# Kernel optimization log

Measured on AMD Instinct MI355X. Metric: run time of the kernel, lower is better.

The kernel has to match this reference:

```python
import jax, jax.numpy as jnp
import numpy as np

HEADS = 24
R = 4          # vae_time_compression_ratio
WIN = 3        # windows_size
PAD_T = R * WIN
ROPE_DIMS = (24, 4, 4)   # mouse_qk_dim_list, sum == head_dim == 32
THETA = 256.0
EPS = 1e-6


def setup_inputs():
    key = jax.random.key(0)
    ks = jax.random.split(key, 8)
    b, tt, th, tw = 2, 16, 30, 52
    C = 768
    head_dim = C // HEADS
    mouse_dim, kb_dim = 2, 6
    nf = (tt - 1) * R + 1          # raw frames so feature_time_dim == tt
    in_mlp = mouse_dim * PAD_T + C
    s = 0.02
    return {
        "mouse_condition": jax.random.normal(ks[0], (b, nf, mouse_dim), jnp.float32),
        "keyboard_condition": jax.random.normal(ks[1], (b, nf, kb_dim), jnp.float32),
        "x": jax.random.normal(ks[2], (b, tt * th * tw, C), jnp.float32),
        "mlp_w1": jax.random.normal(ks[3], (in_mlp, in_mlp), jnp.float32) * s,
        "mlp_b1": jnp.zeros((in_mlp,), jnp.float32),
        "mlp_w2": jax.random.normal(ks[4], (in_mlp, C), jnp.float32) * s,
        "mlp_b2": jnp.zeros((C,), jnp.float32),
        "qkv_w": jax.random.normal(ks[5], (C, 3 * C), jnp.float32) * s,
        "q_gamma": jnp.ones((head_dim,), jnp.float32),
        "k_gamma": jnp.ones((head_dim,), jnp.float32),
        "proj_w": jax.random.normal(ks[6], (C, C), jnp.float32) * s,
        "tt": 16, "th": 30, "tw": 52,
    }


def _rms_norm(x, gamma):
    return x * jax.lax.rsqrt(jnp.mean(x * x, -1, keepdims=True) + EPS) * gamma


def _rope_freqs(tt, head_dim):
    # 3-axis rope, rope_sizes = (tt, 1, 1): axes 1 and 2 have position 0 (identity).
    pos = [jnp.arange(tt, dtype=jnp.float32),
           jnp.zeros(tt, jnp.float32),
           jnp.zeros(tt, jnp.float32)]
    cos_l, sin_l = [], []
    for d, p in zip(ROPE_DIMS, pos):
        freqs = 1.0 / (THETA ** (jnp.arange(0, d, 2, dtype=jnp.float32) / d))
        ang = jnp.outer(p, freqs)                      # (tt, d//2)
        cos_l.append(jnp.repeat(jnp.cos(ang), 2, axis=1))   # interleaved convention
        sin_l.append(jnp.repeat(jnp.sin(ang), 2, axis=1))
    return jnp.concatenate(cos_l, -1), jnp.concatenate(sin_l, -1)  # (tt, head_dim)


def _rotate_half(x):
    xr = x.reshape(*x.shape[:-1], -1, 2)
    return jnp.stack([-xr[..., 1], xr[..., 0]], -1).reshape(x.shape)


def reference(mouse_condition, keyboard_condition, x, mlp_w1, mlp_b1, mlp_w2, mlp_b2,
              qkv_w, q_gamma, k_gamma, proj_w, tt, th, tw):
    b, L, C = x.shape
    S = th * tw
    head_dim = C // HEADS
    md = mouse_condition.shape[-1]

    # 'B (T S) C -> (B S) T C'
    hs = x.reshape(b, tt, S, C).transpose(0, 2, 1, 3).reshape(b * S, tt, C)

    # sliding windows over front-padded mouse signal: stride R, window PAD_T
    mp = jnp.pad(mouse_condition, ((0, 0), (PAD_T, 0), (0, 0)))
    idx = R * jnp.arange(tt)[:, None] + jnp.arange(PAD_T)[None, :]
    gm = mp[:, idx, :].reshape(b, 1, tt, PAD_T * md)          # (window, d) flattened
    gm = jnp.broadcast_to(gm, (b, S, tt, PAD_T * md)).reshape(b * S, tt, PAD_T * md)

    z = jnp.concatenate([hs, gm], -1)
    h = jax.nn.gelu(z @ mlp_w1 + mlp_b1, approximate=True)    # gelu_tanh
    feat = h @ mlp_w2 + mlp_b2                                # (b*S, tt, C)

    qkv = (feat @ qkv_w).reshape(b * S, tt, 3, HEADS, head_dim)
    q, k, v = qkv[:, :, 0], qkv[:, :, 1], qkv[:, :, 2]
    q = _rms_norm(q, q_gamma)
    k = _rms_norm(k, k_gamma)

    cos, sin = _rope_freqs(tt, head_dim)
    cos = cos[None, :, None, :]
    sin = sin[None, :, None, :]
    q = q * cos + _rotate_half(q) * sin
    k = k * cos + _rotate_half(k) * sin

    scale = head_dim ** -0.5
    scores = jnp.einsum('blhd,bmhd->bhlm', q, k) * scale
    p = jax.nn.softmax(scores, axis=-1)
    attn = jnp.einsum('bhlm,bmhd->blhd', p, v).reshape(b * S, tt, C)

    # '(b S) T h d -> b (T S) (h d)'
    attn = attn.reshape(b, S, tt, C).transpose(0, 2, 1, 3).reshape(b, tt * S, C)
    return x + attn @ proj_w
```

## Files before the change

### kernel.cpp

```cpp
#include <hip/hip_runtime.h>

typedef unsigned short u16;
typedef __bf16 bf16x8 __attribute__((ext_vector_type(8)));
typedef float f32x4 __attribute__((ext_vector_type(4)));
typedef short short8 __attribute__((ext_vector_type(8)));

#define TT 16
#define SP 1560
#define CDIM 768
#define NHEADS 24
#define KP 800
#define HROWS 896
#define HSTR 800

__device__ __forceinline__ float b2f(u16 u){
  unsigned int x = ((unsigned int)u) << 16;
  return __builtin_bit_cast(float, x);
}
__device__ __forceinline__ u16 f2b(float f){
  unsigned int x = __builtin_bit_cast(unsigned int, f);
  x += 0x7fffu + ((x >> 16) & 1u);
  return (u16)(x >> 16);
}
__device__ __forceinline__ float ldf(const void* p, size_t i, int f32){
  return f32 ? ((const float*)p)[i] : b2f(((const u16*)p)[i]);
}
__device__ __forceinline__ void g2l16(const void* g, void* l){
  __builtin_amdgcn_global_load_lds((const __attribute__((address_space(1))) void*)g,
                                   (__attribute__((address_space(3))) void*)l, 16, 0, 0);
}

__global__ void detect_dtype(const u16* __restrict__ x, int* __restrict__ flag){
  __shared__ int sh[256];
  int tid = threadIdx.x;
  int cnt = 0;
  #pragma unroll
  for (int j=0;j<8;j++){
    u16 u = x[(size_t)(tid*8+j)*2];
    int e = (u >> 7) & 0xff;
    cnt += (e >= 90 && e <= 160) ? 1 : 0;
  }
  sh[tid] = cnt;
  __syncthreads();
  if (tid == 0){
    int s = 0;
    for (int k=0;k<256;k++) s += sh[k];
    *flag = (s < 1024) ? 1 : 0;
  }
}

__global__ void convert(const void* __restrict__ src, u16* __restrict__ dst,
                        int n, const int* __restrict__ flagp){
  int f = *flagp;
  int i = blockIdx.x*256 + threadIdx.x;
  int stride = gridDim.x*256;
  if (f){
    const float* s = (const float*)src;
    for (int j=i; j<n; j+=stride) dst[j] = f2b(s[j]);
  } else {
    const u16* s = (const u16*)src;
    for (int j=i; j<n; j+=stride) dst[j] = s[j];
  }
}

__global__ void build_gm(const void* __restrict__ mouse, u16* __restrict__ gm,
                         int b, const int* __restrict__ flagp){
  int f = *flagp;
  int i = blockIdx.x*256 + threadIdx.x;
  if (i >= b*TT*32) return;
  int col = i & 31, tix = i >> 5;
  int t = tix & 15, bidx = tix >> 4;
  float v = 0.f;
  if (col < 24){
    int j = col >> 1, c = col & 1;
    int p = 4*t + j;
    if (p >= 12) v = ldf(mouse, (size_t)(bidx*61 + (p-12))*2 + c, f);
  }
  gm[i] = f2b(v);
}

__global__ void transpose_pad(const void* __restrict__ src, u16* __restrict__ dst,
                              int K, int N, int Kpad, int Npad,
                              const int* __restrict__ flagp){
  int f = *flagp;
  __shared__ u16 tile[32][33];
  int k0 = blockIdx.x*32, n0 = blockIdx.y*32;
  int tx = threadIdx.x, ty = threadIdx.y;
  #pragma unroll
  for (int i=0;i<32;i+=8){
    int k = k0+ty+i, n = n0+tx;
    u16 v = 0;
    if (k<K && n<N) v = f ? f2b(((const float*)src)[(size_t)k*N+n])
                          : ((const u16*)src)[(size_t)k*N+n];
    tile[ty+i][tx] = v;
  }
  __syncthreads();
  #pragma unroll
  for (int i=0;i<32;i+=8){
    int n = n0+ty+i, k = k0+tx;
    if (n<Npad && k<Kpad) dst[(size_t)n*Kpad+k] = tile[tx][ty+i];
  }
}

template<int AMODE, int EPI>
__global__ __launch_bounds__(256, 4) void gemm(
    const u16* __restrict__ A, int lda,
    const u16* __restrict__ Bt, int ldb, int Kpad,
    const u16* __restrict__ bias,
    const u16* __restrict__ X,
    const u16* __restrict__ gmtab,
    u16* __restrict__ C, u16* __restrict__ Ck, u16* __restrict__ Cv,
    int ldc, int nmax,
    const int* __restrict__ flagp)
{
  __shared__ __attribute__((aligned(16))) u16 As[2][128*32];
  __shared__ __attribute__((aligned(16))) u16 Bs[2][128*32];
  int f32out = 0;
  if constexpr (EPI==3) f32out = *flagp;

  const int gx = gridDim.x;
  const int nwg = gx * gridDim.y;
  const int orig = blockIdx.y * gx + blockIdx.x;
  const int q8 = nwg >> 3, r8 = nwg & 7;
  const int xcd = orig & 7, idx = orig >> 3;
  const int nl = (xcd < r8 ? xcd*(q8+1) : r8*(q8+1) + (xcd-r8)*q8) + idx;
  const int bx = nl % gx, by = nl / gx;

  const int tid = threadIdx.x;
  const int wave = tid >> 6, lane = tid & 63;
  const int lrow = lane & 15, quad = lane >> 4;
  const int m0 = by * 128, n0 = bx * 128;
  const int wm = (wave >> 1) * 64, wn = (wave & 1) * 64;
  const int row = tid >> 2;
  const int kc  = (tid & 3) << 3;

  f32x4 acc[4][4];
  #pragma unroll
  for (int r=0;r<4;r++)
    #pragma unroll
    for (int c=0;c<4;c++) acc[r][c] = (f32x4){0.f,0.f,0.f,0.f};

  auto STAGE = [&](int bi, int k0){
    #pragma unroll
    for (int ch=0; ch<2; ch++){
      int m = m0 + ch*64 + row;
      const u16* srcA;
      if (AMODE==1 && k0 >= CDIM) srcA = gmtab + (m/SP)*32 + (k0 - CDIM) + kc;
      else                        srcA = A + (size_t)m*lda + k0 + kc;
      g2l16(srcA, (char*)(&As[bi][0]) + ch*4096 + wave*1024);
      int n = n0 + ch*64 + row;
      const u16* srcB = Bt + (size_t)n*ldb + k0 + kc;
      g2l16(srcB, (char*)(&Bs[bi][0]) + ch*4096 + wave*1024);
    }
  };

  auto COMPUTE = [&](int bi){
    bf16x8 af[4], bfr[4];
    #pragma unroll
    for (int r=0;r<4;r++) af[r]  = *(const bf16x8*)&As[bi][(wm + r*16 + lrow)*32 + quad*8];
    #pragma unroll
    for (int c=0;c<4;c++) bfr[c] = *(const bf16x8*)&Bs[bi][(wn + c*16 + lrow)*32 + quad*8];
    #pragma unroll
    for (int r=0;r<4;r++)
      #pragma unroll
      for (int c=0;c<4;c++)
        acc[r][c] = __builtin_amdgcn_mfma_f32_16x16x32_bf16(af[r], bfr[c], acc[r][c], 0, 0, 0);
  };

  const int nt = Kpad >> 5;
  STAGE(0, 0);
  __syncthreads();
  int cur = 0;
  for (int t = 0; t < nt-1; ++t){
    STAGE(cur^1, (t+1) << 5);
    COMPUTE(cur);
    __syncthreads();
    cur ^= 1;
  }
  COMPUTE(cur);

  #pragma unroll
  for (int c=0;c<4;c++){
    int n = n0 + wn + c*16 + lrow;
    float bv = 0.f;
    if (EPI==1) bv = (n < 792) ? b2f(bias[n]) : 0.f;
    if (EPI==2) bv = b2f(bias[n]);
    u16* dstb = C;
    int nn = n;
    if constexpr (EPI==4){
      int sec = n / 768;
      nn = n - sec*768;
      dstb = (sec==0) ? C : ((sec==1) ? Ck : Cv);
    }
    #pragma unroll
    for (int r=0;r<4;r++){
      #pragma unroll
      for (int i=0;i<4;i++){
        int m = m0 + wm + r*16 + quad*4 + i;
        float v = acc[r][c][i] + bv;
        if (EPI==1){
          float u = 0.7978845608028654f*(v + 0.044715f*v*v*v);
          v = 0.5f*v*(1.f + tanhf(u));
        }
        if (EPI==3) v += b2f(X[(size_t)m*CDIM + n]);
        if (n < nmax){
          if constexpr (EPI==3){
            if (f32out) ((float*)C)[(size_t)m*ldc + n] = v;
            else        C[(size_t)m*ldc + n] = f2b(v);
          } else {
            dstb[(size_t)m*ldc + nn] = f2b(v);
          }
        }
      }
    }
  }
}

__global__ __launch_bounds__(256) void attn_kernel(
    const u16* __restrict__ qp, const u16* __restrict__ kp,
    const u16* __restrict__ vp, const u16* __restrict__ qg,
    const u16* __restrict__ kg, u16* __restrict__ outp)
{
  __shared__ float qs[4][16][32];
  __shared__ float ks[4][16][32];
  __shared__ float vs[4][16][32];
  __shared__ float ps[4][16][16];
  const int tid = threadIdx.x;
  const int wave = tid >> 6, lane = tid & 63;
  const int inst = blockIdx.x*4 + wave;
  const int head = inst % NHEADS;
  const int bs   = inst / NHEADS;
  const int s = bs % SP, bidx = bs / SP;
  const int t = lane >> 2, ch = lane & 3;
  const size_t mrow = (size_t)(bidx*TT + t)*SP + s;
  const size_t off = mrow*CDIM + head*32 + ch*8;

  float qf[8], kf[8], vf[8];
  {
    short8 r0 = *(const short8*)(qp + off);
    short8 r1 = *(const short8*)(kp + off);
    short8 r2 = *(const short8*)(vp + off);
    #pragma unroll
    for (int j=0;j<8;j++){ qf[j]=b2f((u16)r0[j]); kf[j]=b2f((u16)r1[j]); vf[j]=b2f((u16)r2[j]); }
  }
  float ssq=0.f, ssk=0.f;
  #pragma unroll
  for (int j=0;j<8;j++){ ssq += qf[j]*qf[j]; ssk += kf[j]*kf[j]; }
  ssq += __shfl_xor(ssq,1); ssq += __shfl_xor(ssq,2);
  ssk += __shfl_xor(ssk,1); ssk += __shfl_xor(ssk,2);
  float rq = rsqrtf(ssq*(1.f/32.f) + 1e-6f);
  float rk = rsqrtf(ssk*(1.f/32.f) + 1e-6f);
  #pragma unroll
  for (int j=0;j<8;j++){
    int d = ch*8 + j;
    qf[j] *= rq * b2f(qg[d]);
    kf[j] *= rk * b2f(kg[d]);
  }
  #pragma unroll
  for (int u=0;u<4;u++){
    int p = ch*4 + u;
    if (p < 12){
      float ang = (float)t * exp2f(-0.66666667f * (float)p);
      float sn, cs;
      __sincosf(ang, &sn, &cs);
      float a=qf[2*u], b=qf[2*u+1];
      qf[2*u]   = a*cs - b*sn;
      qf[2*u+1] = b*cs + a*sn;
      a=kf[2*u]; b=kf[2*u+1];
      kf[2*u]   = a*cs - b*sn;
      kf[2*u+1] = b*cs + a*sn;
    }
  }
  #pragma unroll
  for (int j=0;j<8;j++){
    qs[wave][t][ch*8+j]=qf[j];
    ks[wave][t][ch*8+j]=kf[j];
    vs[wave][t][ch*8+j]=vf[j];
  }
  __syncthreads();
  float sc[4]; float mx = -3.4e38f;
  #pragma unroll
  for (int jj=0;jj<4;jj++){
    int j = ch*4 + jj;
    float d = 0.f;
    #pragma unroll
    for (int dd=0;dd<32;dd++) d += qs[wave][t][dd]*ks[wave][j][dd];
    sc[jj] = d * 0.17677669529663689f;
    mx = fmaxf(mx, sc[jj]);
  }
  mx = fmaxf(mx, __shfl_xor(mx,1)); mx = fmaxf(mx, __shfl_xor(mx,2));
  float sum=0.f; float ex[4];
  #pragma unroll
  for (int jj=0;jj<4;jj++){ ex[jj]=__expf(sc[jj]-mx); sum+=ex[jj]; }
  sum += __shfl_xor(sum,1); sum += __shfl_xor(sum,2);
  float inv = 1.f/sum;
  #pragma unroll
  for (int jj=0;jj<4;jj++) ps[wave][t][ch*4+jj] = ex[jj]*inv;
  __syncthreads();
  float o[8] = {0,0,0,0,0,0,0,0};
  #pragma unroll
  for (int j=0;j<16;j++){
    float p = ps[wave][t][j];
    #pragma unroll
    for (int dd=0;dd<8;dd++) o[dd] += p * vs[wave][j][ch*8+dd];
  }
  union { short8 v; u16 u[8]; } pk;
  #pragma unroll
  for (int dd=0;dd<8;dd++) pk.u[dd] = f2b(o[dd]);
  *(short8*)(outp + off) = pk.v;
}

extern "C" void kernel_launch(void* const* d_in, const int* in_sizes, int n_in,
                              void* d_out, int out_size, void* d_ws, size_t ws_size,
                              hipStream_t stream){
  const void* mouse = d_in[0];
  const void* x     = d_in[2];
  const void* w1    = d_in[3];
  const void* b1    = d_in[4];
  const void* w2    = d_in[5];
  const void* b2    = d_in[6];
  const void* qkvw  = d_in[7];
  const void* qg    = d_in[8];
  const void* kg    = d_in[9];
  const void* projw = d_in[10];
  const int b = in_sizes[0] / (61*2);
  const int M = b * TT * SP;

  u16* ws    = (u16*)d_ws;
  int* flag  = (int*)ws;
  u16* gm    = ws + 32;
  u16* bcvt  = gm + 1024;
  u16* b1b   = bcvt;
  u16* b2b   = bcvt + 800;
  u16* qgb   = bcvt + 1568;
  u16* kgb   = bcvt + 1600;
  u16* w1t   = bcvt + 2048;
  u16* w2t   = w1t  + (size_t)HROWS*KP;
  u16* qkvt  = w2t  + (size_t)CDIM*KP;
  u16* projt = qkvt + (size_t)(3*CDIM)*CDIM;
  u16* xb    = projt+ (size_t)CDIM*CDIM;
  u16* h     = xb   + (size_t)M*CDIM;
  u16* feat  = h    + (size_t)M*HSTR;
  u16* kbuf  = feat + (size_t)M*CDIM;
  u16* vbuf  = kbuf + (size_t)M*CDIM;
  u16* qbuf  = h;
  u16* attn  = feat;

  detect_dtype<<<1, 256, 0, stream>>>((const u16*)x, flag);
  convert<<<dim3(4),    256, 0, stream>>>(b1, b1b, 792, flag);
  convert<<<dim3(3),    256, 0, stream>>>(b2, b2b, 768, flag);
  convert<<<dim3(1),    256, 0, stream>>>(qg, qgb, 32, flag);
  convert<<<dim3(1),    256, 0, stream>>>(kg, kgb, 32, flag);
  convert<<<dim3(8192), 256, 0, stream>>>(x,  xb,  M*CDIM, flag);
  build_gm<<<dim3((b*TT*32+255)/256), 256, 0, stream>>>(mouse, gm, b, flag);
  dim3 tb(32,8);
  transpose_pad<<<dim3(KP/32,   HROWS/32),    tb, 0, stream>>>(w1,   w1t,   792,  792,    KP,   HROWS, flag);
  transpose_pad<<<dim3(KP/32,   CDIM/32),     tb, 0, stream>>>(w2,   w2t,   792,  CDIM,   KP,   CDIM,  flag);
  transpose_pad<<<dim3(CDIM/32, (3*CDIM)/32), tb, 0, stream>>>(qkvw, qkvt,  CDIM, 3*CDIM, CDIM, 3*CDIM,flag);
  transpose_pad<<<dim3(CDIM/32, CDIM/32),     tb, 0, stream>>>(projw, projt, CDIM, CDIM,  CDIM, CDIM,  flag);

  gemm<1,1><<<dim3(HROWS/128, M/128), 256, 0, stream>>>(xb,   CDIM, w1t,  KP,   KP,   b1b, nullptr, gm,
                                                        h,    nullptr, nullptr, HSTR, 800, flag);
  gemm<0,2><<<dim3(CDIM/128,  M/128), 256, 0, stream>>>(h,    HSTR, w2t,  KP,   KP,   b2b, nullptr, nullptr,
                                                        feat, nullptr, nullptr, CDIM, 768, flag);
  gemm<0,4><<<dim3((3*CDIM)/128, M/128), 256, 0, stream>>>(feat, CDIM, qkvt, CDIM, CDIM, nullptr, nullptr, nullptr,
                                                           qbuf, kbuf, vbuf, CDIM, 3*CDIM, flag);
  attn_kernel<<<dim3(b*SP*NHEADS/4), 256, 0, stream>>>(qbuf, kbuf, vbuf, qgb, kgb, attn);
  gemm<0,3><<<dim3(CDIM/128,  M/128), 256, 0, stream>>>(attn, CDIM, projt, CDIM, CDIM, nullptr, xb, nullptr,
                                                        (u16*)d_out, nullptr, nullptr, CDIM, 768, flag);
}
```

Measured before the change: 1.058 ms.

## Replace 128x128 GEMM with 256x256 tiled, swizzled, phase-pipelined GEMM

Replaces the 128x128x32 double-buffered GEMM with a 512-thread 256x256x64 tile kernel. It uses XOR-swizzled LDS layout, four-phase interleaving of half-tile loads with MFMA work, and setprio around the compute. K padding grows to 896, N padding for the first GEMM to 1024, and the gm table widens to 128 columns to fit the 64-wide K steps. The goal is more data reuse per LDS load and fewer bank conflicts and stalls, at the cost of larger padding waste and lower occupancy.

Result: slower. 1.209 ms (+14.2%).

```diff
diff --git a/kernel.cpp b/kernel.cpp
--- a/kernel.cpp
+++ b/kernel.cpp
@@ -9,9 +9,9 @@
 #define SP 1560
 #define CDIM 768
 #define NHEADS 24
-#define KP 800
-#define HROWS 896
-#define HSTR 800
+#define KP1 896
+#define HSTR 896
+#define N1PAD 1024
 
 __device__ __forceinline__ float b2f(u16 u){
   unsigned int x = ((unsigned int)u) << 16;
@@ -67,8 +67,8 @@
                          int b, const int* __restrict__ flagp){
   int f = *flagp;
   int i = blockIdx.x*256 + threadIdx.x;
-  if (i >= b*TT*32) return;
-  int col = i & 31, tix = i >> 5;
+  if (i >= b*TT*128) return;
+  int col = i & 127, tix = i >> 7;
   int t = tix & 15, bidx = tix >> 4;
   float v = 0.f;
   if (col < 24){
@@ -103,7 +103,7 @@
 }
 
 template<int AMODE, int EPI>
-__global__ __launch_bounds__(256, 4) void gemm(
+__global__ __launch_bounds__(512, 2) void gemm256(
     const u16* __restrict__ A, int lda,
     const u16* __restrict__ Bt, int ldb, int Kpad,
     const u16* __restrict__ bias,
@@ -113,10 +113,8 @@
     int ldc, int nmax,
     const int* __restrict__ flagp)
 {
-  __shared__ __attribute__((aligned(16))) u16 As[2][128*32];
-  __shared__ __attribute__((aligned(16))) u16 Bs[2][128*32];
-  int f32out = 0;
-  if constexpr (EPI==3) f32out = *flagp;
+  __shared__ __attribute__((aligned(16))) u16 sA[2][256*64];
+  __shared__ __attribute__((aligned(16))) u16 sB[2][256*64];
 
   const int gx = gridDim.x;
   const int nwg = gx * gridDim.y;
@@ -128,60 +126,109 @@
 
   const int tid = threadIdx.x;
   const int wave = tid >> 6, lane = tid & 63;
-  const int lrow = lane & 15, quad = lane >> 4;
-  const int m0 = by * 128, n0 = bx * 128;
-  const int wm = (wave >> 1) * 64, wn = (wave & 1) * 64;
-  const int row = tid >> 2;
-  const int kc  = (tid & 3) << 3;
-
-  f32x4 acc[4][4];
-  #pragma unroll
-  for (int r=0;r<4;r++)
+  const int wm8 = wave >> 2, wn8 = wave & 3;
+  const int lrow = lane & 15, hi16 = lane >> 4;
+  const int m0 = by*256, n0 = bx*256;
+
+  f32x4 acc[8][4];
+  #pragma unroll
+  for (int r=0;r<8;r++)
     #pragma unroll
     for (int c=0;c<4;c++) acc[r][c] = (f32x4){0.f,0.f,0.f,0.f};
 
-  auto STAGE = [&](int bi, int k0){
-    #pragma unroll
-    for (int ch=0; ch<2; ch++){
-      int m = m0 + ch*64 + row;
-      const u16* srcA;
-      if (AMODE==1 && k0 >= CDIM) srcA = gmtab + (m/SP)*32 + (k0 - CDIM) + kc;
-      else                        srcA = A + (size_t)m*lda + k0 + kc;
-      g2l16(srcA, (char*)(&As[bi][0]) + ch*4096 + wave*1024);
-      int n = n0 + ch*64 + row;
-      const u16* srcB = Bt + (size_t)n*ldb + k0 + kc;
-      g2l16(srcB, (char*)(&Bs[bi][0]) + ch*4096 + wave*1024);
+  const int nt = Kpad >> 6;
+  const int niter = nt >> 1;
+
+  auto STAGE = [&](int isB, int buf, int half, int k0){
+    #pragma unroll
+    for (int is=0; is<2; is++){
+      int r = half*128 + is*64 + (tid>>3);
+      int ck = (((tid&7) ^ (r&7)) << 3);
+      const u16* src;
+      if (isB){
+        src = Bt + (size_t)(n0 + r)*ldb + k0 + ck;
+      } else {
+        int m = m0 + r;
+        if (AMODE==1 && k0 >= CDIM) src = gmtab + (size_t)(m/SP)*128 + (k0 - CDIM) + ck;
+        else                        src = A + (size_t)m*lda + k0 + ck;
+      }
+      char* l = (char*)(isB ? &sB[buf][0] : &sA[buf][0]) + half*16384 + is*8192 + wave*1024;
+      g2l16(src, l);
     }
   };
 
-  auto COMPUTE = [&](int bi){
-    bf16x8 af[4], bfr[4];
-    #pragma unroll
-    for (int r=0;r<4;r++) af[r]  = *(const bf16x8*)&As[bi][(wm + r*16 + lrow)*32 + quad*8];
-    #pragma unroll
-    for (int c=0;c<4;c++) bfr[c] = *(const bf16x8*)&Bs[bi][(wn + c*16 + lrow)*32 + quad*8];
-    #pragma unroll
-    for (int r=0;r<4;r++)
+  bf16x8 bfr[8];
+  auto LDB_ALL = [&](int buf){
+    #pragma unroll
+    for (int nn=0; nn<4; nn++){
+      int r = wn8*64 + nn*16 + lrow;
       #pragma unroll
-      for (int c=0;c<4;c++)
-        acc[r][c] = __builtin_amdgcn_mfma_f32_16x16x32_bf16(af[r], bfr[c], acc[r][c], 0, 0, 0);
+      for (int ks=0; ks<2; ks++){
+        int o = (r<<7) + (ks<<6) + (hi16<<4);
+        o ^= (r&7)<<4;
+        bfr[nn*2+ks] = *(const bf16x8*)((const char*)&sB[buf][0] + o);
+      }
+    }
   };
 
-  const int nt = Kpad >> 5;
-  STAGE(0, 0);
-  __syncthreads();
-  int cur = 0;
-  for (int t = 0; t < nt-1; ++t){
-    STAGE(cur^1, (t+1) << 5);
-    COMPUTE(cur);
-    __syncthreads();
-    cur ^= 1;
-  }
-  COMPUTE(cur);
-
-  #pragma unroll
-  for (int c=0;c<4;c++){
-    int n = n0 + wn + c*16 + lrow;
+  auto PHASE = [&](int q, int buf, int sIsB, int sbuf, int shalf, int sk0, int vm_end){
+    bf16x8 a[4];
+    #pragma unroll
+    for (int mm=0; mm<2; mm++){
+      int r = wm8*128 + (q*2+mm)*16 + lrow;
+      #pragma unroll
+      for (int ks=0; ks<2; ks++){
+        int o = (r<<7) + (ks<<6) + (hi16<<4);
+        o ^= (r&7)<<4;
+        a[mm*2+ks] = *(const bf16x8*)((const char*)&sA[buf][0] + o);
+      }
+    }
+    if (q==0) LDB_ALL(buf);
+    STAGE(sIsB, sbuf, shalf, sk0);
+    __builtin_amdgcn_s_barrier();
+    asm volatile("s_waitcnt lgkmcnt(0)" ::: "memory");
+    __builtin_amdgcn_sched_barrier(0);
+    __builtin_amdgcn_s_setprio(1);
+    #pragma unroll
+    for (int mm=0; mm<2; mm++)
+      #pragma unroll
+      for (int nf=0; nf<4; nf++)
+        #pragma unroll
+        for (int ks=0; ks<2; ks++)
+          acc[q*2+mm][nf] = __builtin_amdgcn_mfma_f32_16x16x32_bf16(
+              a[mm*2+ks], bfr[nf*2+ks], acc[q*2+mm][nf], 0, 0, 0);
+    __builtin_amdgcn_s_setprio(0);
+    if (vm_end) asm volatile("s_waitcnt vmcnt(4)" ::: "memory");
+    __builtin_amdgcn_s_barrier();
+  };
+
+  STAGE(1,0,0,0); STAGE(1,0,1,0);
+  STAGE(0,0,0,0); STAGE(0,0,1,0);
+  STAGE(1,1,0,64); STAGE(1,1,1,64);
+  asm volatile("s_waitcnt vmcnt(4)" ::: "memory");
+  __builtin_amdgcn_s_barrier();
+
+  for (int i=0; i<niter; ++i){
+    int kA1 = (2*i+1) << 6;
+    int t2 = 2*i+2; if (t2 > nt-1) t2 = nt-1;
+    int t3 = 2*i+3; if (t3 > nt-1) t3 = nt-1;
+    int k2 = t2 << 6, k3 = t3 << 6;
+    PHASE(0, 0, 0, 1, 0, kA1, 0);
+    PHASE(1, 0, 0, 1, 1, kA1, 0);
+    PHASE(2, 0, 1, 0, 0, k2,  0);
+    PHASE(3, 0, 1, 0, 1, k2,  1);
+    PHASE(0, 1, 0, 0, 0, k2,  0);
+    PHASE(1, 1, 0, 0, 1, k2,  0);
+    PHASE(2, 1, 1, 1, 0, k3,  0);
+    PHASE(3, 1, 1, 1, 1, k3,  1);
+  }
+  asm volatile("s_waitcnt vmcnt(0)" ::: "memory");
+
+  int f32out = 0;
+  if constexpr (EPI==3) f32out = *flagp;
+  #pragma unroll
+  for (int nf=0; nf<4; nf++){
+    int n = n0 + wn8*64 + nf*16 + lrow;
     float bv = 0.f;
     if (EPI==1) bv = (n < 792) ? b2f(bias[n]) : 0.f;
     if (EPI==2) bv = b2f(bias[n]);
@@ -193,11 +240,11 @@
       dstb = (sec==0) ? C : ((sec==1) ? Ck : Cv);
     }
     #pragma unroll
-    for (int r=0;r<4;r++){
+    for (int mf=0; mf<8; mf++){
       #pragma unroll
-      for (int i=0;i<4;i++){
-        int m = m0 + wm + r*16 + quad*4 + i;
-        float v = acc[r][c][i] + bv;
+      for (int i2=0; i2<4; i2++){
+        int m = m0 + wm8*128 + mf*16 + hi16*4 + i2;
+        float v = acc[mf][nf][i2] + bv;
         if (EPI==1){
           float u = 0.7978845608028654f*(v + 0.044715f*v*v*v);
           v = 0.5f*v*(1.f + tanhf(u));
@@ -329,14 +376,14 @@
   u16* ws    = (u16*)d_ws;
   int* flag  = (int*)ws;
   u16* gm    = ws + 32;
-  u16* bcvt  = gm + 1024;
+  u16* bcvt  = gm + (size_t)b*TT*128;
   u16* b1b   = bcvt;
   u16* b2b   = bcvt + 800;
   u16* qgb   = bcvt + 1568;
   u16* kgb   = bcvt + 1600;
   u16* w1t   = bcvt + 2048;
-  u16* w2t   = w1t  + (size_t)HROWS*KP;
-  u16* qkvt  = w2t  + (size_t)CDIM*KP;
+  u16* w2t   = w1t  + (size_t)N1PAD*KP1;
+  u16* qkvt  = w2t  + (size_t)CDIM*KP1;
   u16* projt = qkvt + (size_t)(3*CDIM)*CDIM;
   u16* xb    = projt+ (size_t)CDIM*CDIM;
   u16* h     = xb   + (size_t)M*CDIM;
@@ -352,20 +399,20 @@
   convert<<<dim3(1),    256, 0, stream>>>(qg, qgb, 32, flag);
   convert<<<dim3(1),    256, 0, stream>>>(kg, kgb, 32, flag);
   convert<<<dim3(8192), 256, 0, stream>>>(x,  xb,  M*CDIM, flag);
-  build_gm<<<dim3((b*TT*32+255)/256), 256, 0, stream>>>(mouse, gm, b, flag);
+  build_gm<<<dim3((b*TT*128+255)/256), 256, 0, stream>>>(mouse, gm, b, flag);
   dim3 tb(32,8);
-  transpose_pad<<<dim3(KP/32,   HROWS/32),    tb, 0, stream>>>(w1,   w1t,   792,  792,    KP,   HROWS, flag);
-  transpose_pad<<<dim3(KP/32,   CDIM/32),     tb, 0, stream>>>(w2,   w2t,   792,  CDIM,   KP,   CDIM,  flag);
+  transpose_pad<<<dim3(KP1/32,  N1PAD/32),    tb, 0, stream>>>(w1,   w1t,   792,  792,    KP1,  N1PAD, flag);
+  transpose_pad<<<dim3(KP1/32,  CDIM/32),     tb, 0, stream>>>(w2,   w2t,   792,  CDIM,   KP1,  CDIM,  flag);
   transpose_pad<<<dim3(CDIM/32, (3*CDIM)/32), tb, 0, stream>>>(qkvw, qkvt,  CDIM, 3*CDIM, CDIM, 3*CDIM,flag);
   transpose_pad<<<dim3(CDIM/32, CDIM/32),     tb, 0, stream>>>(projw, projt, CDIM, CDIM,  CDIM, CDIM,  flag);
 
-  gemm<1,1><<<dim3(HROWS/128, M/128), 256, 0, stream>>>(xb,   CDIM, w1t,  KP,   KP,   b1b, nullptr, gm,
-                                                        h,    nullptr, nullptr, HSTR, 800, flag);
-  gemm<0,2><<<dim3(CDIM/128,  M/128), 256, 0, stream>>>(h,    HSTR, w2t,  KP,   KP,   b2b, nullptr, nullptr,
-                                                        feat, nullptr, nullptr, CDIM, 768, flag);
-  gemm<0,4><<<dim3((3*CDIM)/128, M/128), 256, 0, stream>>>(feat, CDIM, qkvt, CDIM, CDIM, nullptr, nullptr, nullptr,
-                                                           qbuf, kbuf, vbuf, CDIM, 3*CDIM, flag);
+  gemm256<1,1><<<dim3(N1PAD/256, M/256), 512, 0, stream>>>(xb,  CDIM, w1t, KP1, KP1, b1b, nullptr, gm,
+                                                           h,   nullptr, nullptr, HSTR, 896, flag);
+  gemm256<0,2><<<dim3(CDIM/256,  M/256), 512, 0, stream>>>(h,   HSTR, w2t, KP1, KP1, b2b, nullptr, nullptr,
+                                                           feat, nullptr, nullptr, CDIM, 768, flag);
+  gemm256<0,4><<<dim3((3*CDIM)/256, M/256), 512, 0, stream>>>(feat, CDIM, qkvt, CDIM, CDIM, nullptr, nullptr, nullptr,
+                                                              qbuf, kbuf, vbuf, CDIM, 3*CDIM, flag);
   attn_kernel<<<dim3(b*SP*NHEADS/4), 256, 0, stream>>>(qbuf, kbuf, vbuf, qgb, kgb, attn);
-  gemm<0,3><<<dim3(CDIM/128,  M/128), 256, 0, stream>>>(attn, CDIM, projt, CDIM, CDIM, nullptr, xb, nullptr,
-                                                        (u16*)d_out, nullptr, nullptr, CDIM, 768, flag);
-}
+  gemm256<0,3><<<dim3(CDIM/256,  M/256), 512, 0, stream>>>(attn, CDIM, projt, CDIM, CDIM, nullptr, xb, nullptr,
+                                                           (u16*)d_out, nullptr, nullptr, CDIM, 768, flag);
+}
```

## Add triple-buffered swizzled QKV GEMM and LDS-staged vectorized epilogue stores

Applied to the files above, without the earlier changes.

Adds a dedicated QKV projection GEMM with 512 threads and 128x256 tiles. It triple-buffers LDS with an XOR swizzle to avoid bank conflicts, interleaves MFMA with async global-to-LDS loads, and uses explicit barriers, waitcnts and setprio. The generic GEMM epilogue now stages bf16 results through shared memory and writes them out as 16-byte vector stores instead of scattered 2-byte stores. The fp32 output path of the projection GEMM keeps direct stores. The cost is higher LDS use and register pressure, plus fragile hand-written synchronization in the new pipelined loop.

Result: faster. 942.2 us (-11.0%).

```diff
diff --git a/kernel.cpp b/kernel.cpp
--- a/kernel.cpp
+++ b/kernel.cpp
@@ -103,18 +103,16 @@
 }
 
 template<int AMODE, int EPI>
-__global__ __launch_bounds__(256, 4) void gemm(
+__global__ __launch_bounds__(256, 4) void gemm128(
     const u16* __restrict__ A, int lda,
     const u16* __restrict__ Bt, int ldb, int Kpad,
     const u16* __restrict__ bias,
     const u16* __restrict__ X,
     const u16* __restrict__ gmtab,
-    u16* __restrict__ C, u16* __restrict__ Ck, u16* __restrict__ Cv,
-    int ldc, int nmax,
+    u16* __restrict__ C, int ldc, int nmax,
     const int* __restrict__ flagp)
 {
-  __shared__ __attribute__((aligned(16))) u16 As[2][128*32];
-  __shared__ __attribute__((aligned(16))) u16 Bs[2][128*32];
+  __shared__ __attribute__((aligned(16))) u16 smem[16384];
   int f32out = 0;
   if constexpr (EPI==3) f32out = *flagp;
 
@@ -147,19 +145,21 @@
       const u16* srcA;
       if (AMODE==1 && k0 >= CDIM) srcA = gmtab + (m/SP)*32 + (k0 - CDIM) + kc;
       else                        srcA = A + (size_t)m*lda + k0 + kc;
-      g2l16(srcA, (char*)(&As[bi][0]) + ch*4096 + wave*1024);
+      g2l16(srcA, (char*)smem + bi*8192 + ch*4096 + wave*1024);
       int n = n0 + ch*64 + row;
       const u16* srcB = Bt + (size_t)n*ldb + k0 + kc;
-      g2l16(srcB, (char*)(&Bs[bi][0]) + ch*4096 + wave*1024);
+      g2l16(srcB, (char*)smem + 16384 + bi*8192 + ch*4096 + wave*1024);
     }
   };
 
   auto COMPUTE = [&](int bi){
     bf16x8 af[4], bfr[4];
     #pragma unroll
-    for (int r=0;r<4;r++) af[r]  = *(const bf16x8*)&As[bi][(wm + r*16 + lrow)*32 + quad*8];
-    #pragma unroll
-    for (int c=0;c<4;c++) bfr[c] = *(const bf16x8*)&Bs[bi][(wn + c*16 + lrow)*32 + quad*8];
+    for (int r=0;r<4;r++)
+      af[r]  = *(const bf16x8*)((const char*)smem + bi*8192 + (wm + r*16 + lrow)*64 + quad*16);
+    #pragma unroll
+    for (int c=0;c<4;c++)
+      bfr[c] = *(const bf16x8*)((const char*)smem + 16384 + bi*8192 + (wn + c*16 + lrow)*64 + quad*16);
     #pragma unroll
     for (int r=0;r<4;r++)
       #pragma unroll
@@ -178,40 +178,190 @@
     cur ^= 1;
   }
   COMPUTE(cur);
-
+  __syncthreads();
+
+  if constexpr (EPI==3){
+    if (f32out){
+      #pragma unroll
+      for (int c=0;c<4;c++){
+        int n = n0 + wn + c*16 + lrow;
+        #pragma unroll
+        for (int r=0;r<4;r++){
+          #pragma unroll
+          for (int i=0;i<4;i++){
+            int m = m0 + wm + r*16 + quad*4 + i;
+            float v = acc[r][c][i] + b2f(X[(size_t)m*CDIM + n]);
+            if (n < nmax) ((float*)C)[(size_t)m*ldc + n] = v;
+          }
+        }
+      }
+      return;
+    }
+  }
   #pragma unroll
   for (int c=0;c<4;c++){
     int n = n0 + wn + c*16 + lrow;
     float bv = 0.f;
     if (EPI==1) bv = (n < 792) ? b2f(bias[n]) : 0.f;
     if (EPI==2) bv = b2f(bias[n]);
-    u16* dstb = C;
-    int nn = n;
-    if constexpr (EPI==4){
-      int sec = n / 768;
-      nn = n - sec*768;
-      dstb = (sec==0) ? C : ((sec==1) ? Ck : Cv);
-    }
     #pragma unroll
     for (int r=0;r<4;r++){
       #pragma unroll
       for (int i=0;i<4;i++){
-        int m = m0 + wm + r*16 + quad*4 + i;
+        int rw = wm + r*16 + quad*4 + i;
         float v = acc[r][c][i] + bv;
         if (EPI==1){
           float u = 0.7978845608028654f*(v + 0.044715f*v*v*v);
           v = 0.5f*v*(1.f + tanhf(u));
         }
-        if (EPI==3) v += b2f(X[(size_t)m*CDIM + n]);
-        if (n < nmax){
-          if constexpr (EPI==3){
-            if (f32out) ((float*)C)[(size_t)m*ldc + n] = v;
-            else        C[(size_t)m*ldc + n] = f2b(v);
-          } else {
-            dstb[(size_t)m*ldc + nn] = f2b(v);
-          }
-        }
+        if (EPI==3) v += b2f(X[(size_t)(m0+rw)*CDIM + n]);
+        smem[rw*128 + (wn + c*16 + lrow)] = f2b(v);
       }
+    }
+  }
+  __syncthreads();
+  {
+    int colu = (tid & 15) * 8;
+    int n = n0 + colu;
+    if (n < nmax){
+      #pragma unroll
+      for (int j=0;j<8;j++){
+        int rw = (tid >> 4) + j*16;
+        short8 vv = *(const short8*)&smem[rw*128 + colu];
+        *(short8*)&C[(size_t)(m0+rw)*ldc + n] = vv;
+      }
+    }
+  }
+}
+
+__global__ __launch_bounds__(512, 4) void gemm_qkv(
+    const u16* __restrict__ A, int lda,
+    const u16* __restrict__ Bt, int ldb, int Kpad,
+    u16* __restrict__ C, u16* __restrict__ Ck, u16* __restrict__ Cv,
+    int ldc)
+{
+  __shared__ __attribute__((aligned(16))) u16 smem[36864];
+
+  const int gx = gridDim.x;
+  const int nwg = gx * gridDim.y;
+  const int orig = blockIdx.y * gx + blockIdx.x;
+  const int q8 = nwg >> 3, r8 = nwg & 7;
+  const int xcd = orig & 7, idx = orig >> 3;
+  const int nl = (xcd < r8 ? xcd*(q8+1) : r8*(q8+1) + (xcd-r8)*q8) + idx;
+  const int bx = nl % gx, by = nl / gx;
+
+  const int tid = threadIdx.x;
+  const int wave = tid >> 6, lane = tid & 63;
+  const int wmh = wave >> 2, wnq = wave & 3;
+  const int lrow = lane & 15, hi16 = lane >> 4;
+  const int m0 = by*128, n0 = bx*256;
+
+  f32x4 acc[4][4];
+  #pragma unroll
+  for (int r=0;r<4;r++)
+    #pragma unroll
+    for (int c=0;c<4;c++) acc[r][c] = (f32x4){0.f,0.f,0.f,0.f};
+
+  const int srow = tid >> 2;
+  const int schk = tid & 3;
+
+  auto STAGE_A = [&](int buf, int k0){
+    int ck = ((schk ^ ((srow>>1)&3)) << 3);
+    const u16* src = A + (size_t)(m0 + srow)*lda + k0 + ck;
+    g2l16(src, (char*)smem + buf*8192 + wave*1024);
+  };
+  auto STAGE_B = [&](int buf, int half, int k0){
+    int r = half*128 + srow;
+    int ck = ((schk ^ ((r>>1)&3)) << 3);
+    const u16* src = Bt + (size_t)(n0 + r)*ldb + k0 + ck;
+    g2l16(src, (char*)smem + 24576 + buf*16384 + half*8192 + wave*1024);
+  };
+  auto LDA = [&](int buf, int mf)->bf16x8{
+    int r = wmh*64 + mf*16 + lrow;
+    int o = r*64 + ((hi16 ^ ((r>>1)&3))<<4);
+    return *(const bf16x8*)((const char*)smem + buf*8192 + o);
+  };
+  auto LDB = [&](int buf, int nf)->bf16x8{
+    int r = wnq*64 + nf*16 + lrow;
+    int o = r*64 + ((hi16 ^ ((r>>1)&3))<<4);
+    return *(const bf16x8*)((const char*)smem + 24576 + buf*16384 + o);
+  };
+
+  const int nt = Kpad >> 5;
+  STAGE_A(0, 0);  STAGE_B(0,0,0);  STAGE_B(0,1,0);
+  STAGE_A(1, 32); STAGE_B(1,0,32); STAGE_B(1,1,32);
+  asm volatile("s_waitcnt vmcnt(3)" ::: "memory");
+  __builtin_amdgcn_s_barrier();
+
+  int buf = 0;
+  for (int t = 0; t < nt; ++t){
+    int ts = t+2; if (ts > nt-1) ts = nt-1;
+    int ks = ts << 5;
+    int nbuf = buf+2; if (nbuf >= 3) nbuf -= 3;
+    bf16x8 a0 = LDA(buf,0), a1 = LDA(buf,1);
+    bf16x8 b0 = LDB(buf,0), b1 = LDB(buf,1), b2v = LDB(buf,2), b3 = LDB(buf,3);
+    STAGE_A(nbuf, ks);
+    STAGE_B(nbuf, 0, ks);
+    __builtin_amdgcn_s_barrier();
+    asm volatile("s_waitcnt lgkmcnt(0)" ::: "memory");
+    __builtin_amdgcn_sched_barrier(0);
+    __builtin_amdgcn_s_setprio(1);
+    acc[0][0] = __builtin_amdgcn_mfma_f32_16x16x32_bf16(a0, b0, acc[0][0], 0,0,0);
+    acc[0][1] = __builtin_amdgcn_mfma_f32_16x16x32_bf16(a0, b1, acc[0][1], 0,0,0);
+    acc[0][2] = __builtin_amdgcn_mfma_f32_16x16x32_bf16(a0, b2v, acc[0][2], 0,0,0);
+    acc[0][3] = __builtin_amdgcn_mfma_f32_16x16x32_bf16(a0, b3, acc[0][3], 0,0,0);
+    acc[1][0] = __builtin_amdgcn_mfma_f32_16x16x32_bf16(a1, b0, acc[1][0], 0,0,0);
+    acc[1][1] = __builtin_amdgcn_mfma_f32_16x16x32_bf16(a1, b1, acc[1][1], 0,0,0);
+    acc[1][2] = __builtin_amdgcn_mfma_f32_16x16x32_bf16(a1, b2v, acc[1][2], 0,0,0);
+    acc[1][3] = __builtin_amdgcn_mfma_f32_16x16x32_bf16(a1, b3, acc[1][3], 0,0,0);
+    __builtin_amdgcn_s_setprio(0);
+    __builtin_amdgcn_s_barrier();
+    bf16x8 a2 = LDA(buf,2), a3 = LDA(buf,3);
+    STAGE_B(nbuf, 1, ks);
+    __builtin_amdgcn_s_barrier();
+    asm volatile("s_waitcnt lgkmcnt(0)" ::: "memory");
+    __builtin_amdgcn_sched_barrier(0);
+    __builtin_amdgcn_s_setprio(1);
+    acc[2][0] = __builtin_amdgcn_mfma_f32_16x16x32_bf16(a2, b0, acc[2][0], 0,0,0);
+    acc[2][1] = __builtin_amdgcn_mfma_f32_16x16x32_bf16(a2, b1, acc[2][1], 0,0,0);
+    acc[2][2] = __builtin_amdgcn_mfma_f32_16x16x32_bf16(a2, b2v, acc[2][2], 0,0,0);
+    acc[2][3] = __builtin_amdgcn_mfma_f32_16x16x32_bf16(a2, b3, acc[2][3], 0,0,0);
+    acc[3][0] = __builtin_amdgcn_mfma_f32_16x16x32_bf16(a3, b0, acc[3][0], 0,0,0);
+    acc[3][1] = __builtin_amdgcn_mfma_f32_16x16x32_bf16(a3, b1, acc[3][1], 0,0,0);
+    acc[3][2] = __builtin_amdgcn_mfma_f32_16x16x32_bf16(a3, b2v, acc[3][2], 0,0,0);
+    acc[3][3] = __builtin_amdgcn_mfma_f32_16x16x32_bf16(a3, b3, acc[3][3], 0,0,0);
+    __builtin_amdgcn_s_setprio(0);
+    asm volatile("s_waitcnt vmcnt(3)" ::: "memory");
+    __builtin_amdgcn_s_barrier();
+    buf = (buf+1 == 3) ? 0 : buf+1;
+  }
+  asm volatile("s_waitcnt vmcnt(0)" ::: "memory");
+  __syncthreads();
+
+  #pragma unroll
+  for (int nf=0; nf<4; nf++){
+    int col = wnq*64 + nf*16 + lrow;
+    #pragma unroll
+    for (int mf=0; mf<4; mf++){
+      #pragma unroll
+      for (int i2=0; i2<4; i2++){
+        int rw = wmh*64 + mf*16 + hi16*4 + i2;
+        smem[rw*256 + col] = f2b(acc[mf][nf][i2]);
+      }
+    }
+  }
+  __syncthreads();
+  {
+    int colu = (tid & 31) * 8;
+    int n = n0 + colu;
+    int sec = n0 / 768;
+    int nn = n - sec*768;
+    u16* dstb = (sec==0) ? C : ((sec==1) ? Ck : Cv);
+    #pragma unroll
+    for (int j=0;j<8;j++){
+      int rw = (tid >> 5) + j*16;
+      short8 vv = *(const short8*)&smem[rw*256 + colu];
+      *(short8*)&dstb[(size_t)(m0+rw)*ldc + nn] = vv;
     }
   }
 }
@@ -359,13 +509,13 @@
   transpose_pad<<<dim3(CDIM/32, (3*CDIM)/32), tb, 0, stream>>>(qkvw, qkvt,  CDIM, 3*CDIM, CDIM, 3*CDIM,flag);
   transpose_pad<<<dim3(CDIM/32, CDIM/32),     tb, 0, stream>>>(projw, projt, CDIM, CDIM,  CDIM, CDIM,  flag);
 
-  gemm<1,1><<<dim3(HROWS/128, M/128), 256, 0, stream>>>(xb,   CDIM, w1t,  KP,   KP,   b1b, nullptr, gm,
-                                                        h,    nullptr, nullptr, HSTR, 800, flag);
-  gemm<0,2><<<dim3(CDIM/128,  M/128), 256, 0, stream>>>(h,    HSTR, w2t,  KP,   KP,   b2b, nullptr, nullptr,
-                                                        feat, nullptr, nullptr, CDIM, 768, flag);
-  gemm<0,4><<<dim3((3*CDIM)/128, M/128), 256, 0, stream>>>(feat, CDIM, qkvt, CDIM, CDIM, nullptr, nullptr, nullptr,
-                                                           qbuf, kbuf, vbuf, CDIM, 3*CDIM, flag);
+  gemm128<1,1><<<dim3(HROWS/128, M/128), 256, 0, stream>>>(xb, CDIM, w1t, KP, KP, b1b, nullptr, gm,
+                                                           h, HSTR, 800, flag);
+  gemm128<0,2><<<dim3(CDIM/128,  M/128), 256, 0, stream>>>(h, HSTR, w2t, KP, KP, b2b, nullptr, nullptr,
+                                                           feat, CDIM, 768, flag);
+  gemm_qkv<<<dim3((3*CDIM)/256, M/128), 512, 0, stream>>>(feat, CDIM, qkvt, CDIM, CDIM,
+                                                          qbuf, kbuf, vbuf, CDIM);
   attn_kernel<<<dim3(b*SP*NHEADS/4), 256, 0, stream>>>(qbuf, kbuf, vbuf, qgb, kgb, attn);
-  gemm<0,3><<<dim3(CDIM/128,  M/128), 256, 0, stream>>>(attn, CDIM, projt, CDIM, CDIM, nullptr, xb, nullptr,
-                                                        (u16*)d_out, nullptr, nullptr, CDIM, 768, flag);
-}
+  gemm128<0,3><<<dim3(CDIM/128,  M/128), 256, 0, stream>>>(attn, CDIM, projt, CDIM, CDIM, nullptr, xb, nullptr,
+                                                           (u16*)d_out, CDIM, 768, flag);
+}
```
